# Kernel optimization log

Hardware: AMD Instinct MI355X
Metric: run time of the kernel (lower is better)

Reference implementation:

```python
import jax, jax.numpy as jnp
import numpy as np

STYLE_DIM = 512
NUM_DOMAINS = 8
BATCH = 16384
N_DEC_LAYERS = 4
N_EXP_LAYERS = 4   # each expert: Linear+ReLU x3, then Linear


def setup_inputs() -> dict:
    key = jax.random.key(0)
    ks = jax.random.split(key, 6)
    D, E, B = STYLE_DIM, NUM_DOMAINS, BATCH
    scale = 1.0 / np.sqrt(D)  # ~ torch Linear default init scale
    s = jax.random.normal(ks[0], (B, D), dtype=jnp.float32)
    y = jax.random.randint(ks[1], (B,), 0, E, dtype=jnp.int32)
    # decomposer params: stacked [L, out, in] / [L, out]
    dec_W = jax.random.uniform(ks[2], (N_DEC_LAYERS, D, D), jnp.float32, -scale, scale)
    dec_b = jax.random.uniform(ks[3], (N_DEC_LAYERS, D), jnp.float32, -scale, scale)
    # expert params: stacked [E, L, out, in] / [E, L, out]
    exp_W = jax.random.uniform(ks[4], (E, N_EXP_LAYERS, D, D), jnp.float32, -scale, scale)
    exp_b = jax.random.uniform(ks[5], (E, N_EXP_LAYERS, D), jnp.float32, -scale, scale)
    return {"s": s, "y": y, "dec_W": dec_W, "dec_b": dec_b, "exp_W": exp_W, "exp_b": exp_b}


def reference(s, y, dec_W, dec_b, exp_W, exp_b):
    h = s
    for l in range(N_DEC_LAYERS):
        h = jax.nn.relu(jnp.einsum('bi,oi->bo', h, dec_W[l]) + dec_b[l])
    s_unrelated = h                      # [B, D]
    s_related = s - s_unrelated          # [B, D]

    # run ALL experts on every sample (faithful to original dense compute)
    x = jnp.broadcast_to(s_related[:, None, :], (s.shape[0], NUM_DOMAINS, s.shape[1]))
    for l in range(N_EXP_LAYERS):
        x = jnp.einsum('bei,eoi->beo', x, exp_W[:, l]) + exp_b[:, l]
        if l < N_EXP_LAYERS - 1:
            x = jax.nn.relu(x)
    # gather the per-sample domain output: out[idx, y]
    s_related_tilde = jnp.take_along_axis(x, y[:, None, None].astype(jnp.int32), axis=1)[:, 0, :]
    s_tilde = s_related_tilde + s_unrelated
    return s_tilde
```

## Files before the change

### kernel.cpp

```cpp
#include <hip/hip_runtime.h>
#include <stdint.h>

#define BB 16384
#define PR2 16896
#define MAXT2 264

typedef short bf16x8 __attribute__((ext_vector_type(8)));
typedef float f32x4 __attribute__((ext_vector_type(4)));
typedef unsigned short us4v __attribute__((ext_vector_type(4)));

typedef __attribute__((address_space(1))) unsigned short gus_t;
typedef __attribute__((address_space(3))) unsigned short lus_t;

__device__ __forceinline__ unsigned short f2bf(float f) {
    unsigned int u = __float_as_uint(f);
    u += 0x7fffu + ((u >> 16) & 1u);
    return (unsigned short)(u >> 16);
}
__device__ __forceinline__ float bf2f(unsigned short h) {
    return __uint_as_float(((unsigned int)h) << 16);
}

__device__ __forceinline__ void gld16(const unsigned short* g, unsigned short* l) {
    __builtin_amdgcn_global_load_lds(
        reinterpret_cast<const gus_t*>(reinterpret_cast<uintptr_t>(g)),
        reinterpret_cast<lus_t*>(reinterpret_cast<uintptr_t>(l)),
        16, 0, 0);
}

__global__ void cvt_bf16(const float* __restrict__ src, unsigned short* __restrict__ dst, int n4) {
    int stride = gridDim.x * blockDim.x;
    for (int i = blockIdx.x * blockDim.x + threadIdx.x; i < n4; i += stride) {
        f32x4 v = reinterpret_cast<const f32x4*>(src)[i];
        us4v o;
        o[0] = f2bf(v[0]); o[1] = f2bf(v[1]); o[2] = f2bf(v[2]); o[3] = f2bf(v[3]);
        reinterpret_cast<us4v*>(dst)[i] = o;
    }
}

__global__ void bucket_init(int* perm, int* counts, int* cursors, int* tile_exp) {
    int i = blockIdx.x * blockDim.x + threadIdx.x;
    if (i < PR2) perm[i] = -1;
    if (i < 8) { counts[i] = 0; cursors[i] = 0; }
    if (i < MAXT2) tile_exp[i] = 0;
}

__global__ __launch_bounds__(1024) void bucket_count(const int* __restrict__ y, int* counts) {
    __shared__ int lc[8];
    const int t = threadIdx.x;
    if (t < 8) lc[t] = 0;
    __syncthreads();
    atomicAdd(&lc[y[blockIdx.x * 1024 + t]], 1);
    __syncthreads();
    if (t < 8) atomicAdd(&counts[t], lc[t]);
}

__global__ void bucket_scan(const int* __restrict__ counts, int* starts, int* tile_exp) {
    if (threadIdx.x == 0 && blockIdx.x == 0) {
        int s = 0;
        for (int e = 0; e < 8; ++e) {
            starts[e] = s;
            int nt = (counts[e] + 63) >> 6;
            for (int t = 0; t < nt; ++t) tile_exp[(s >> 6) + t] = e;
            s += nt << 6;
        }
        starts[8] = s;
    }
}

__global__ __launch_bounds__(1024) void bucket_scatter(const int* __restrict__ y,
                                                       const int* __restrict__ starts,
                                                       int* cursors, int* perm) {
    __shared__ int lc[8];
    __shared__ int lbase[8];
    const int t = threadIdx.x;
    if (t < 8) lc[t] = 0;
    __syncthreads();
    const int i = blockIdx.x * 1024 + t;
    const int e = y[i];
    const int r = atomicAdd(&lc[e], 1);
    __syncthreads();
    if (t < 8) lbase[t] = atomicAdd(&cursors[t], lc[t]);
    __syncthreads();
    perm[starts[e] + lbase[e] + r] = i;
}

#define STAGE(x_) do {                                                        \
    const unsigned short* wp_ = Wl + (((size_t)((x_) >> 4)) << 18)            \
        + ((size_t)((((x_) & 15) + off) & 15) << 5) + wsrc_off;               \
    unsigned short* ld_ = wdst0 + (((x_) % 3) << 11);                         \
    gld16(wp_,         ld_);                                                  \
    gld16(wp_ +  8192, ld_ +  512);                                           \
    gld16(wp_ + 16384, ld_ + 1024);                                           \
    gld16(wp_ + 24576, ld_ + 1536);                                           \
} while (0)

template <int PHASE>
__global__ __launch_bounds__(512) void fused4(
    const float* __restrict__ sf32,
    const unsigned short* __restrict__ srelg,
    const unsigned short* __restrict__ Wb,
    const float* __restrict__ biasb,
    unsigned short* __restrict__ srel_out,
    unsigned short* __restrict__ h_out,
    const unsigned short* __restrict__ h_in,
    float* __restrict__ outf,
    const int* __restrict__ perm,
    const int* __restrict__ tile_exp,
    const int* __restrict__ starts8)
{
    __shared__ __align__(16) unsigned short ls[81920];

    const int bid = blockIdx.x;
    int tile;
    if (PHASE == 0) {
        tile = ((bid & 7) << 5) + (bid >> 3);
    } else {
        tile = (bid & 7) * 33 + (bid >> 3);
        if ((tile << 6) >= starts8[0]) return;
    }

    const unsigned short* Wl;
    const float* bl;
    if (PHASE == 0) { Wl = Wb; bl = biasb; }
    else {
        const int e = tile_exp[tile];
        Wl = Wb + ((size_t)e << 20);
        bl = biasb + (e << 11);
    }

    const int t = threadIdx.x;
    const int w = t >> 6;
    const int lane = t & 63;
    const int lr = lane & 15;
    const int kg = lane >> 4;
    const int off = ((tile * 3) + w) & 15;

    const int asrc_c = (t & 56) | ((t ^ (t >> 6)) & 7);
    const int axor = lr & 7;
    int arow_e[4];
#pragma unroll
    for (int m = 0; m < 4; ++m) arow_e[m] = ((m << 4) + lr) << 9;

    const int wcb = w << 6;
    const size_t wsrc_off = (((size_t)(wcb + (lane >> 2))) << 9) + ((lane & 3) << 3);
    unsigned short* const wdst0 = ls + 32768 + w * 6144 + (lane << 3);
    const int wrd0 = 32768 + w * 6144 + (lr << 5) + (kg << 3);

    float bball[16];
#pragma unroll
    for (int l = 0; l < 4; ++l)
#pragma unroll
        for (int j = 0; j < 4; ++j)
            bball[(l << 2) + j] = bl[(l << 9) + (w << 6) + (j << 4) + lr];
    asm volatile("s_waitcnt vmcnt(0)" ::: "memory");

    if (PHASE == 0) {
#pragma unroll
        for (int c8 = 0; c8 < 8; ++c8) {
            const int grow = (tile << 6) + (c8 << 3) + w;
            const float* sp = sf32 + (((size_t)grow) << 9) + (asrc_c << 3);
            f32x4 v0 = *reinterpret_cast<const f32x4*>(sp);
            f32x4 v1 = *reinterpret_cast<const f32x4*>(sp + 4);
            bf16x8 o;
#pragma unroll
            for (int q = 0; q < 4; ++q) { o[q] = (short)f2bf(v0[q]); o[q + 4] = (short)f2bf(v1[q]); }
            *reinterpret_cast<bf16x8*>(&ls[(c8 << 12) + (t << 3)]) = o;
        }
        asm volatile("s_waitcnt lgkmcnt(0)" ::: "memory");
    } else {
#pragma unroll
        for (int c8 = 0; c8 < 8; ++c8) {
            int pr = perm[(tile << 6) + (c8 << 3) + w];
            if (pr < 0) pr = 0;
            gld16(srelg + (((size_t)pr) << 9) + (asrc_c << 3), ls + (c8 << 12) + (t << 3));
        }
        asm volatile("s_waitcnt vmcnt(0)" ::: "memory");
    }
    STAGE(0);
    STAGE(1);
    __builtin_amdgcn_s_barrier();

    f32x4 acc[4][4];
#pragma unroll
    for (int m = 0; m < 4; ++m)
#pragma unroll
        for (int j = 0; j < 4; ++j)
            acc[m][j] = f32x4{0.f, 0.f, 0.f, 0.f};

    for (int s = 0; s < 64; ++s) {
        if (s < 63) asm volatile("s_waitcnt vmcnt(4)" ::: "memory");
        else        asm volatile("s_waitcnt vmcnt(0)" ::: "memory");
        if (s + 2 < 64) STAGE(s + 2);

        const int st = ((s & 15) + off) & 15;
        const int sb = (st >> 1) << 6;
        const int klo = ((((st & 1) << 2) | kg) ^ axor) << 3;
        const int wb = (s % 3) << 11;
        bf16x8 af[4], bv[4];
#pragma unroll
        for (int m = 0; m < 4; ++m)
            af[m] = *reinterpret_cast<const bf16x8*>(&ls[arow_e[m] + sb + klo]);
#pragma unroll
        for (int j = 0; j < 4; ++j)
            bv[j] = *reinterpret_cast<const bf16x8*>(&ls[wrd0 + wb + (j << 9)]);
        __builtin_amdgcn_s_setprio(1);
#pragma unroll
        for (int m = 0; m < 4; ++m)
#pragma unroll
            for (int j = 0; j < 4; ++j)
                acc[m][j] = __builtin_amdgcn_mfma_f32_16x16x32_bf16(af[m], bv[j], acc[m][j], 0, 0, 0);
        __builtin_amdgcn_s_setprio(0);

        if ((s & 15) == 15 && s < 63) {
            __builtin_amdgcn_s_barrier();
            asm volatile("" ::: "memory");
            const int lbb = (s >> 4) << 2;
#pragma unroll
            for (int m = 0; m < 4; ++m)
#pragma unroll
                for (int j = 0; j < 4; ++j) {
#pragma unroll
                    for (int reg = 0; reg < 4; ++reg) {
                        const int row = (m << 4) + (kg << 2) + reg;
                        const float v = fmaxf(acc[m][j][reg] + bball[lbb + j], 0.f);
                        const int swc = (w << 3) + (((j << 1) + (lr >> 3)) ^ (row & 7));
                        ls[(row << 9) + (swc << 3) + (lr & 7)] = f2bf(v);
                    }
                    acc[m][j] = f32x4{0.f, 0.f, 0.f, 0.f};
                }
            asm volatile("s_waitcnt lgkmcnt(0)" ::: "memory");
            __builtin_amdgcn_s_barrier();
            asm volatile("" ::: "memory");
        }
    }

    if (PHASE == 0) {
        __syncthreads();
#pragma unroll
        for (int m = 0; m < 4; ++m)
#pragma unroll
            for (int j = 0; j < 4; ++j)
#pragma unroll
                for (int reg = 0; reg < 4; ++reg) {
                    const int row = (m << 4) + (kg << 2) + reg;
                    const int col = (w << 6) + (j << 4) + lr;
                    const float h = fmaxf(acc[m][j][reg] + bball[12 + j], 0.f);
                    const float sv = sf32[(((size_t)((tile << 6) + row)) << 9) + col];
                    const int swc = (w << 3) + (((j << 1) + (lr >> 3)) ^ (row & 7));
                    const int idx = (row << 9) + (swc << 3) + (lr & 7);
                    ls[idx] = f2bf(sv - h);
                    ls[32768 + idx] = f2bf(h);
                }
        __syncthreads();
#pragma unroll
        for (int c8 = 0; c8 < 8; ++c8) {
            const int row = (c8 << 3) + w;
            const size_t go = (((size_t)((tile << 6) + row)) << 9) + (asrc_c << 3);
            bf16x8 va = *reinterpret_cast<const bf16x8*>(&ls[(c8 << 12) + (t << 3)]);
            bf16x8 vh = *reinterpret_cast<const bf16x8*>(&ls[32768 + (c8 << 12) + (t << 3)]);
            *reinterpret_cast<bf16x8*>(&srel_out[go]) = va;
            *reinterpret_cast<bf16x8*>(&h_out[go]) = vh;
        }
    } else {
#pragma unroll
        for (int m = 0; m < 4; ++m) {
#pragma unroll
            for (int reg = 0; reg < 4; ++reg) {
                const int row = (m << 4) + (kg << 2) + reg;
                const int pr = perm[(tile << 6) + row];
                if (pr >= 0) {
#pragma unroll
                    for (int j = 0; j < 4; ++j) {
                        const int col = (w << 6) + (j << 4) + lr;
                        const size_t gi = (((size_t)pr) << 9) + col;
                        outf[gi] = acc[m][reg >> 2 == 0 ? j : j][reg] + bball[12 + j] + bf2f(h_in[gi]);
                    }
                }
            }
        }
    }
}

extern "C" void kernel_launch(void* const* d_in, const int* in_sizes, int n_in,
                              void* d_out, int out_size, void* d_ws, size_t ws_size,
                              hipStream_t stream)
{
    const float* s     = (const float*)d_in[0];
    const int*   y     = (const int*)d_in[1];
    const float* dec_W = (const float*)d_in[2];
    const float* dec_b = (const float*)d_in[3];
    const float* exp_W = (const float*)d_in[4];
    const float* exp_b = (const float*)d_in[5];
    float* out = (float*)d_out;

    unsigned short* decWb = (unsigned short*)d_ws;
    unsigned short* expWb = decWb + 4 * 512 * 512;
    unsigned short* srel  = expWb + 8 * 4 * 512 * 512;
    unsigned short* hbuf  = srel + (size_t)BB * 512;
    int* perm     = (int*)(hbuf + (size_t)BB * 512);
    int* counts   = perm + PR2;
    int* cursors  = counts + 8;
    int* starts   = cursors + 8;
    int* tile_exp = starts + 9;

    cvt_bf16<<<256, 256, 0, stream>>>(dec_W, decWb, (4 * 512 * 512) / 4);
    cvt_bf16<<<2048, 256, 0, stream>>>(exp_W, expWb, (8 * 4 * 512 * 512) / 4);

    bucket_init<<<(PR2 + 255) / 256, 256, 0, stream>>>(perm, counts, cursors, tile_exp);
    bucket_count<<<BB / 1024, 1024, 0, stream>>>(y, counts);
    bucket_scan<<<1, 64, 0, stream>>>(counts, starts, tile_exp);
    bucket_scatter<<<BB / 1024, 1024, 0, stream>>>(y, starts, cursors, perm);

    fused4<0><<<256, 512, 0, stream>>>(s, nullptr, decWb, dec_b, srel, hbuf,
                                       nullptr, nullptr, nullptr, nullptr, nullptr);
    fused4<1><<<MAXT2, 512, 0, stream>>>(nullptr, srel, expWb, exp_b, nullptr, nullptr,
                                         hbuf, out, perm, tile_exp, starts + 8);
}
```

Measured before the change: 182.9 us.

## Software-pipeline LDS fragment reads and swizzle weight staging in fused MLP kernel

Restructures the main K loop so the LDS fragments for the next step are read into alternate register sets (double buffering) while the current step's MFMAs run. The initial weight staging is also overlapped with loading the activation tile. A rotated swizzle on weight column groups is meant to cut LDS bank conflicts on the B-fragment reads. The cost is more live vector registers and tighter waitcnt bookkeeping, which could reduce occupancy or cause register spills.

```diff
diff --git a/kernel.cpp b/kernel.cpp
--- a/kernel.cpp
+++ b/kernel.cpp
@@ -84,16 +84,6 @@
     __syncthreads();
     perm[starts[e] + lbase[e] + r] = i;
 }
-
-#define STAGE(x_) do {                                                        \
-    const unsigned short* wp_ = Wl + (((size_t)((x_) >> 4)) << 18)            \
-        + ((size_t)((((x_) & 15) + off) & 15) << 5) + wsrc_off;               \
-    unsigned short* ld_ = wdst0 + (((x_) % 3) << 11);                         \
-    gld16(wp_,         ld_);                                                  \
-    gld16(wp_ +  8192, ld_ +  512);                                           \
-    gld16(wp_ + 16384, ld_ + 1024);                                           \
-    gld16(wp_ + 24576, ld_ + 1536);                                           \
-} while (0)
 
 template <int PHASE>
 __global__ __launch_bounds__(512) void fused4(
@@ -143,9 +133,44 @@
     for (int m = 0; m < 4; ++m) arow_e[m] = ((m << 4) + lr) << 9;
 
     const int wcb = w << 6;
-    const size_t wsrc_off = (((size_t)(wcb + (lane >> 2))) << 9) + ((lane & 3) << 3);
-    unsigned short* const wdst0 = ls + 32768 + w * 6144 + (lane << 3);
-    const int wrd0 = 32768 + w * 6144 + (lr << 5) + (kg << 3);
+    int colterm[4];
+#pragma unroll
+    for (int q = 0; q < 4; ++q) {
+        const int cq = (q << 4) + (lane >> 2);
+        const int kgq = ((lane & 3) - (cq >> 1)) & 3;
+        colterm[q] = ((wcb + cq) << 9) + (kgq << 3);
+    }
+    const int wavebase = 32768 + w * 6144;
+    unsigned short* const wdst = ls + wavebase + (lane << 3);
+    const int wrd0e = (lr << 5) + (((kg + (lr >> 1)) & 3) << 3);
+
+#define STAGE(x_, b_) do {                                               \
+    const unsigned short* wp_ = Wl + (((size_t)((x_) >> 4)) << 18)       \
+        + (((((x_) & 15) + off) & 15) << 5);                             \
+    unsigned short* ld_ = wdst + ((b_) << 11);                           \
+    gld16(wp_ + colterm[0], ld_);                                        \
+    gld16(wp_ + colterm[1], ld_ +  512);                                 \
+    gld16(wp_ + colterm[2], ld_ + 1024);                                 \
+    gld16(wp_ + colterm[3], ld_ + 1536);                                 \
+} while (0)
+
+#define READW(dst_, b_) do {                                             \
+    const unsigned short* lw_ = ls + wavebase + ((b_) << 11) + wrd0e;    \
+    dst_[0] = *reinterpret_cast<const bf16x8*>(lw_);                     \
+    dst_[1] = *reinterpret_cast<const bf16x8*>(lw_ +  512);              \
+    dst_[2] = *reinterpret_cast<const bf16x8*>(lw_ + 1024);              \
+    dst_[3] = *reinterpret_cast<const bf16x8*>(lw_ + 1536);              \
+} while (0)
+
+#define READA(dst_, s1_) do {                                            \
+    const int st_ = (((s1_) & 15) + off) & 15;                           \
+    const int sb_ = (st_ >> 1) << 6;                                     \
+    const int klo_ = ((((st_ & 1) << 2) | kg) ^ axor) << 3;              \
+    dst_[0] = *reinterpret_cast<const bf16x8*>(&ls[arow_e[0] + sb_ + klo_]); \
+    dst_[1] = *reinterpret_cast<const bf16x8*>(&ls[arow_e[1] + sb_ + klo_]); \
+    dst_[2] = *reinterpret_cast<const bf16x8*>(&ls[arow_e[2] + sb_ + klo_]); \
+    dst_[3] = *reinterpret_cast<const bf16x8*>(&ls[arow_e[3] + sb_ + klo_]); \
+} while (0)
 
     float bball[16];
 #pragma unroll
@@ -167,7 +192,11 @@
             for (int q = 0; q < 4; ++q) { o[q] = (short)f2bf(v0[q]); o[q + 4] = (short)f2bf(v1[q]); }
             *reinterpret_cast<bf16x8*>(&ls[(c8 << 12) + (t << 3)]) = o;
         }
+        STAGE(0, 0);
+        STAGE(1, 1);
         asm volatile("s_waitcnt lgkmcnt(0)" ::: "memory");
+        __builtin_amdgcn_s_barrier();
+        asm volatile("s_waitcnt vmcnt(4)" ::: "memory");
     } else {
 #pragma unroll
         for (int c8 = 0; c8 < 8; ++c8) {
@@ -175,11 +204,12 @@
             if (pr < 0) pr = 0;
             gld16(srelg + (((size_t)pr) << 9) + (asrc_c << 3), ls + (c8 << 12) + (t << 3));
         }
-        asm volatile("s_waitcnt vmcnt(0)" ::: "memory");
-    }
-    STAGE(0);
-    STAGE(1);
-    __builtin_amdgcn_s_barrier();
+        STAGE(0, 0);
+        STAGE(1, 1);
+        asm volatile("s_waitcnt vmcnt(8)" ::: "memory");
+        __builtin_amdgcn_s_barrier();
+        asm volatile("s_waitcnt vmcnt(4)" ::: "memory");
+    }
 
     f32x4 acc[4][4];
 #pragma unroll
@@ -188,51 +218,54 @@
         for (int j = 0; j < 4; ++j)
             acc[m][j] = f32x4{0.f, 0.f, 0.f, 0.f};
 
-    for (int s = 0; s < 64; ++s) {
-        if (s < 63) asm volatile("s_waitcnt vmcnt(4)" ::: "memory");
-        else        asm volatile("s_waitcnt vmcnt(0)" ::: "memory");
-        if (s + 2 < 64) STAGE(s + 2);
-
-        const int st = ((s & 15) + off) & 15;
-        const int sb = (st >> 1) << 6;
-        const int klo = ((((st & 1) << 2) | kg) ^ axor) << 3;
-        const int wb = (s % 3) << 11;
-        bf16x8 af[4], bv[4];
-#pragma unroll
-        for (int m = 0; m < 4; ++m)
-            af[m] = *reinterpret_cast<const bf16x8*>(&ls[arow_e[m] + sb + klo]);
-#pragma unroll
-        for (int j = 0; j < 4; ++j)
-            bv[j] = *reinterpret_cast<const bf16x8*>(&ls[wrd0 + wb + (j << 9)]);
-        __builtin_amdgcn_s_setprio(1);
-#pragma unroll
-        for (int m = 0; m < 4; ++m)
-#pragma unroll
-            for (int j = 0; j < 4; ++j)
-                acc[m][j] = __builtin_amdgcn_mfma_f32_16x16x32_bf16(af[m], bv[j], acc[m][j], 0, 0, 0);
-        __builtin_amdgcn_s_setprio(0);
-
-        if ((s & 15) == 15 && s < 63) {
-            __builtin_amdgcn_s_barrier();
-            asm volatile("" ::: "memory");
-            const int lbb = (s >> 4) << 2;
-#pragma unroll
-            for (int m = 0; m < 4; ++m)
-#pragma unroll
-                for (int j = 0; j < 4; ++j) {
-#pragma unroll
-                    for (int reg = 0; reg < 4; ++reg) {
-                        const int row = (m << 4) + (kg << 2) + reg;
-                        const float v = fmaxf(acc[m][j][reg] + bball[lbb + j], 0.f);
-                        const int swc = (w << 3) + (((j << 1) + (lr >> 3)) ^ (row & 7));
-                        ls[(row << 9) + (swc << 3) + (lr & 7)] = f2bf(v);
-                    }
-                    acc[m][j] = f32x4{0.f, 0.f, 0.f, 0.f};
-                }
-            asm volatile("s_waitcnt lgkmcnt(0)" ::: "memory");
-            __builtin_amdgcn_s_barrier();
-            asm volatile("" ::: "memory");
-        }
+    bf16x8 afA[4], bvA[4], afB[4], bvB[4];
+    READA(afA, 0);
+    READW(bvA, 0);
+
+#define ITER(s_, afC, bvC, afN, bvN) do {                                          \
+    if ((s_) + 2 < 64) STAGE((s_) + 2, b2);                                        \
+    if ((s_) < 62) asm volatile("s_waitcnt vmcnt(4)" ::: "memory");                \
+    else           asm volatile("s_waitcnt vmcnt(0)" ::: "memory");                \
+    const bool bnd_ = ((s_) & 15) == 15;                                           \
+    if ((s_) < 63) {                                                               \
+        READW(bvN, b1);                                                            \
+        if (!bnd_) READA(afN, (s_) + 1);                                           \
+    }                                                                              \
+    __builtin_amdgcn_s_setprio(1);                                                 \
+    _Pragma("unroll")                                                              \
+    for (int m = 0; m < 4; ++m)                                                    \
+        _Pragma("unroll")                                                          \
+        for (int j = 0; j < 4; ++j)                                                \
+            acc[m][j] = __builtin_amdgcn_mfma_f32_16x16x32_bf16(afC[m], bvC[j], acc[m][j], 0, 0, 0); \
+    __builtin_amdgcn_s_setprio(0);                                                 \
+    if (bnd_ && (s_) < 63) {                                                       \
+        __builtin_amdgcn_s_barrier();                                              \
+        const int lbb_ = ((s_) >> 4) << 2;                                         \
+        _Pragma("unroll")                                                          \
+        for (int m = 0; m < 4; ++m)                                                \
+            _Pragma("unroll")                                                      \
+            for (int j = 0; j < 4; ++j) {                                          \
+                _Pragma("unroll")                                                  \
+                for (int reg = 0; reg < 4; ++reg) {                                \
+                    const int row_ = (m << 4) + (kg << 2) + reg;                   \
+                    const float v_ = fmaxf(acc[m][j][reg] + bball[lbb_ + j], 0.f); \
+                    const int swc_ = (w << 3) + (((j << 1) + (lr >> 3)) ^ (row_ & 7)); \
+                    ls[(row_ << 9) + (swc_ << 3) + (lr & 7)] = f2bf(v_);           \
+                }                                                                  \
+                acc[m][j] = f32x4{0.f, 0.f, 0.f, 0.f};                             \
+            }                                                                      \
+        asm volatile("s_waitcnt lgkmcnt(0)" ::: "memory");                         \
+        __builtin_amdgcn_s_barrier();                                              \
+        READA(afN, (s_) + 1);                                                      \
+    }                                                                              \
+    b1 = b2; b2 = (b2 + 1 == 3) ? 0 : b2 + 1;                                      \
+} while (0)
+
+    int b1 = 1, b2 = 2;
+    for (int sp = 0; sp < 32; ++sp) {
+        const int s0 = sp << 1;
+        ITER(s0,     afA, bvA, afB, bvB);
+        ITER(s0 + 1, afB, bvB, afA, bvA);
     }
 
     if (PHASE == 0) {
@@ -274,12 +307,16 @@
                     for (int j = 0; j < 4; ++j) {
                         const int col = (w << 6) + (j << 4) + lr;
                         const size_t gi = (((size_t)pr) << 9) + col;
-                        outf[gi] = acc[m][reg >> 2 == 0 ? j : j][reg] + bball[12 + j] + bf2f(h_in[gi]);
+                        outf[gi] = acc[m][j][reg] + bball[12 + j] + bf2f(h_in[gi]);
                     }
                 }
             }
         }
     }
+#undef ITER
+#undef STAGE
+#undef READW
+#undef READA
 }
 
 extern "C" void kernel_launch(void* const* d_in, const int* in_sizes, int n_in,
```

New measurement: 181.4 us. Within noise of the previous version (-0.8%).
